# Optimization experiments

Hardware: AMD Instinct MI355X
Metric: run time of the kernel (lower is better)

Reference implementation:

```python
import jax, jax.numpy as jnp
import numpy as np

B, CI, CO = 16, 16, 16
M1, M2, M3 = 6, 6, 6
NT, NX, NY = 39, 28, 28
NXr, NYr = 14, 14  # int((n-1)/2 + 1) for n=28


def setup_inputs() -> dict:
    key = jax.random.key(0)
    ks = jax.random.split(key, 9)
    scale = 1.0 / (CI * CO)
    u = lambda k, s: scale * jax.random.uniform(k, s, dtype=jnp.float32)
    return {
        "x": jax.random.normal(ks[0], (B, CI, NT, NXr, NYr), dtype=jnp.float32),
        "wp1_re": u(ks[1], (CI, CO, M1)), "wp1_im": u(ks[2], (CI, CO, M1)),
        "wp2_re": u(ks[3], (CI, CO, M2)), "wp2_im": u(ks[4], (CI, CO, M2)),
        "wp3_re": u(ks[5], (CI, CO, M3)), "wp3_im": u(ks[6], (CI, CO, M3)),
        "wr_re": u(ks[7], (CI, CO, M1, M2, M3)), "wr_im": u(ks[8], (CI, CO, M1, M2, M3)),
    }


def _forward(x, wp1, wp2, wp3, wr):
    # grids (match torch.linspace with hardcoded nt/nx/ny and truncation)
    tt_np = np.linspace(0.0, NT - 1, NT)
    tx_np = np.linspace(0.0, 1.0, NX)[:NXr]
    ty_np = np.linspace(0.0, 1.0, NY)[:NYr]
    dtt = float(tt_np[1] - tt_np[0])
    dtx = float(tx_np[1] - tx_np[0])
    dty = float(ty_np[1] - ty_np[0])

    alpha = jnp.fft.fftn(x, axes=(-3, -2, -1))  # [B, CI, NT, NXr, NYr] complex64

    lam1 = (2j * np.pi * jnp.fft.fftfreq(NT, dtt)).astype(jnp.complex64)   # [NT]
    lam2 = (2j * np.pi * jnp.fft.fftfreq(NXr, dtx)).astype(jnp.complex64)  # [NXr]
    lam3 = (2j * np.pi * jnp.fft.fftfreq(NYr, dty)).astype(jnp.complex64)  # [NYr]

    # per-axis pole reciprocals: 1/((l1-p1)(l2-p2)(l3-p3)) = (1/(l1-p1))(1/(l2-p2))(1/(l3-p3))
    r1 = 1.0 / (lam1[:, None, None, None] - wp1[None])  # [NT,  CI, CO, M1]
    r2 = 1.0 / (lam2[:, None, None, None] - wp2[None])  # [NXr, CI, CO, M2]
    r3 = 1.0 / (lam3[:, None, None, None] - wp3[None])  # [NYr, CI, CO, M3]

    # Hw[m,n,l,i,k,p,q,r] = wr[i,k,p,q,r]*r1[m,i,k,p]*r2[n,i,k,q]*r3[l,i,k,r]
    # output_residue1[b,k,m,n,l] = sum_{i,p,q,r} alpha[b,i,m,n,l] * Hw
    or1 = jnp.einsum('bimnl,ikpqr,mikp,nikq,likr->bkmnl', alpha, wr, r1, r2, r3)
    # output_residue2[b,k,p,q,r] = -sum_{i,m,n,l} alpha[b,i,m,n,l] * Hw
    or2 = -jnp.einsum('bimnl,ikpqr,mikp,nikq,likr->bkpqr', alpha, wr, r1, r2, r3)

    x1 = jnp.real(jnp.fft.ifftn(or1, s=(NT, NXr, NYr), axes=(-3, -2, -1))).astype(jnp.float32)

    tt = jnp.asarray(tt_np, dtype=jnp.float32).astype(jnp.complex64)
    tx = jnp.asarray(tx_np, dtype=jnp.float32).astype(jnp.complex64)
    ty = jnp.asarray(ty_np, dtype=jnp.float32).astype(jnp.complex64)

    e1 = jnp.exp(wp1[..., None] * tt)  # [CI, CO, M1, NT]
    e2 = jnp.exp(wp2[..., None] * tx)  # [CI, CO, M2, NXr]
    e3 = jnp.exp(wp3[..., None] * ty)  # [CI, CO, M3, NYr]

    # x2[k,i,z,x,y] = Re( sum_{b,p,q,m} or2[k,b,p,q,m]*e1[b,i,p,z]*e2[b,i,q,x]*e3[b,i,m,y] )
    x2 = jnp.real(jnp.einsum('kbpqm,bipz,biqx,bimy->kizxy', or2, e1, e2, e3)).astype(jnp.float32)
    x2 = x2 / (NT * NXr * NYr)
    return x1 + x2


def reference(x, wp1_re, wp1_im, wp2_re, wp2_im, wp3_re, wp3_im, wr_re, wr_im):
    wp1 = jax.lax.complex(wp1_re, wp1_im)
    wp2 = jax.lax.complex(wp2_re, wp2_im)
    wp3 = jax.lax.complex(wp3_re, wp3_im)
    wr = jax.lax.complex(wr_re, wr_im)
    return _forward(x, wp1, wp2, wp3, wr)
```

## Files before the change

kernel.cpp:

```cpp
#include <hip/hip_runtime.h>

constexpr int kB  = 16;
constexpr int kC  = 16;
constexpr int kM  = 6;
constexpr int kNT = 39;
constexpr int kNX = 14;
constexpr int kNY = 14;
constexpr int kNS = kNX * kNY;
constexpr int kNF = kNT * kNS;
constexpr int kNIK = kC * kC;
constexpr int kMR = kM * kM * kM;
constexpr int kFCH = 6;
constexpr int kVS = 256;

__device__ __forceinline__ float2 cmul(float2 a, float2 b) {
    return make_float2(a.x * b.x - a.y * b.y, a.x * b.y + a.y * b.x);
}
__device__ __forceinline__ void cfma(float2& c, float2 a, float2 b) {
    c.x = fmaf(a.x, b.x, fmaf(-a.y, b.y, c.x));
    c.y = fmaf(a.x, b.y, fmaf(a.y, b.x, c.y));
}

__global__ __launch_bounds__(256) void k_init(
    const float* __restrict__ wp1_re, const float* __restrict__ wp1_im,
    const float* __restrict__ wp2_re, const float* __restrict__ wp2_im,
    const float* __restrict__ wp3_re, const float* __restrict__ wp3_im,
    float2* __restrict__ F39, float2* __restrict__ F14,
    float2* __restrict__ r1t, float2* __restrict__ r2t, float2* __restrict__ r3t,
    float2* __restrict__ e1t, float2* __restrict__ e2t, float2* __restrict__ e3t)
{
    const float PI2 = 6.283185307179586f;
    int tid = blockIdx.x * blockDim.x + threadIdx.x;
    int nth = gridDim.x * blockDim.x;

    for (int idx = tid; idx < kNT * kNT; idx += nth) {
        int m = idx / kNT, t = idx % kNT;
        float ang = -PI2 * (float)((m * t) % kNT) / (float)kNT;
        float s, c; sincosf(ang, &s, &c);
        F39[idx] = make_float2(c, s);
    }
    for (int idx = tid; idx < kNX * kNX; idx += nth) {
        int a = idx / kNX, b = idx % kNX;
        float ang = -PI2 * (float)((a * b) % kNX) / (float)kNX;
        float s, c; sincosf(ang, &s, &c);
        F14[idx] = make_float2(c, s);
    }
    for (int idx = tid; idx < kNIK * kM * kNT; idx += nth) {
        int z = idx % kNT; int ikp = idx / kNT;
        float wre = wp1_re[ikp], wim = wp1_im[ikp];
        float f = (z < 20 ? (float)z : (float)(z - kNT)) / (float)kNT;
        float w = PI2 * f;
        float dr = -wre, di = w - wim;
        float inv = 1.0f / (dr * dr + di * di);
        r1t[idx] = make_float2(dr * inv, -di * inv);
        float tt = (float)z;
        float er = expf(wre * tt);
        float s, c; sincosf(wim * tt, &s, &c);
        e1t[idx] = make_float2(er * c, er * s);
    }
    for (int idx = tid; idx < kNIK * kM * kNX; idx += nth) {
        int n = idx % kNX; int ikq = idx / kNX;
        float f = (n <= 6 ? (float)n : (float)(n - kNX)) * 27.0f / 14.0f;
        float w = PI2 * f;
        float tx = (float)n * (1.0f / 27.0f);
        {
            float wre = wp2_re[ikq], wim = wp2_im[ikq];
            float dr = -wre, di = w - wim;
            float inv = 1.0f / (dr * dr + di * di);
            r2t[idx] = make_float2(dr * inv, -di * inv);
            float er = expf(wre * tx);
            float s, c; sincosf(wim * tx, &s, &c);
            e2t[idx] = make_float2(er * c, er * s);
        }
        {
            float wre = wp3_re[ikq], wim = wp3_im[ikq];
            float dr = -wre, di = w - wim;
            float inv = 1.0f / (dr * dr + di * di);
            r3t[idx] = make_float2(dr * inv, -di * inv);
            float er = expf(wre * tx);
            float s, c; sincosf(wim * tx, &s, &c);
            e3t[idx] = make_float2(er * c, er * s);
        }
    }
}

__global__ __launch_bounds__(256) void k_dft_t_real(
    const float* __restrict__ x, const float2* __restrict__ F39, float2* __restrict__ out)
{
    int bc = blockIdx.x, mg = blockIdx.y;
    __shared__ float2 Fs[13 * kNT];
    int t = threadIdx.x;
    for (int j = t; j < 13 * kNT; j += 256)
        Fs[j] = F39[(mg * 13 + j / kNT) * kNT + (j % kNT)];
    __syncthreads();
    if (t < kNS) {
        float col[kNT];
        const float* xp = x + (size_t)bc * kNF + t;
        #pragma unroll
        for (int tt = 0; tt < kNT; ++tt) col[tt] = xp[(size_t)tt * kNS];
        for (int mi = 0; mi < 13; ++mi) {
            float2 acc = make_float2(0.f, 0.f);
            #pragma unroll
            for (int tt = 0; tt < kNT; ++tt) {
                float2 f = Fs[mi * kNT + tt];
                acc.x = fmaf(f.x, col[tt], acc.x);
                acc.y = fmaf(f.y, col[tt], acc.y);
            }
            out[((size_t)bc * kNT + mg * 13 + mi) * kNS + t] = acc;
        }
    }
}

__global__ __launch_bounds__(256) void k_idft_t(
    const float2* __restrict__ in, const float2* __restrict__ F39, float2* __restrict__ out)
{
    int bk = blockIdx.x, zg = blockIdx.y;
    __shared__ float2 Fs[13 * kNT];
    int t = threadIdx.x;
    for (int j = t; j < 13 * kNT; j += 256) {
        float2 f = F39[(zg * 13 + j / kNT) * kNT + (j % kNT)];
        f.y = -f.y;
        Fs[j] = f;
    }
    __syncthreads();
    if (t < kNS) {
        float2 col[kNT];
        const float2* ip = in + (size_t)bk * kNF + t;
        #pragma unroll
        for (int m = 0; m < kNT; ++m) col[m] = ip[(size_t)m * kNS];
        for (int zi = 0; zi < 13; ++zi) {
            float2 acc = make_float2(0.f, 0.f);
            #pragma unroll
            for (int m = 0; m < kNT; ++m) cfma(acc, Fs[zi * kNT + m], col[m]);
            out[((size_t)bk * kNT + zg * 13 + zi) * kNS + t] = acc;
        }
    }
}

__global__ __launch_bounds__(256) void k_dft_xy(
    const float2* __restrict__ in, const float2* __restrict__ F14, float2* __restrict__ out)
{
    int bm = blockIdx.x;
    __shared__ float2 tile[kNS];
    __shared__ float2 tmp[kNS];
    __shared__ float2 Fs[kNX * kNX];
    int t = threadIdx.x;
    if (t < kNS) tile[t] = in[(size_t)bm * kNS + t];
    if (t < kNX * kNX) Fs[t] = F14[t];
    __syncthreads();
    if (t < kNS) {
        int n2 = t / kNY, l = t % kNY;
        float2 acc = make_float2(0.f, 0.f);
        #pragma unroll
        for (int n = 0; n < kNX; ++n) cfma(acc, Fs[n2 * kNX + n], tile[n * kNY + l]);
        tmp[t] = acc;
    }
    __syncthreads();
    if (t < kNS) {
        int n = t / kNY, l2 = t % kNY;
        float2 acc = make_float2(0.f, 0.f);
        #pragma unroll
        for (int l = 0; l < kNY; ++l) cfma(acc, Fs[l2 * kNY + l], tmp[n * kNY + l]);
        out[(size_t)bm * kNS + t] = acc;
    }
}

__global__ __launch_bounds__(256) void k_idft_xy_final(
    const float2* __restrict__ in, const float2* __restrict__ F14, float* __restrict__ outp)
{
    int bm = blockIdx.x;
    __shared__ float2 tile[kNS];
    __shared__ float2 tmp[kNS];
    __shared__ float2 Fs[kNX * kNX];
    int t = threadIdx.x;
    if (t < kNS) tile[t] = in[(size_t)bm * kNS + t];
    if (t < kNX * kNX) { float2 f = F14[t]; f.y = -f.y; Fs[t] = f; }
    __syncthreads();
    if (t < kNS) {
        int n2 = t / kNY, l = t % kNY;
        float2 acc = make_float2(0.f, 0.f);
        #pragma unroll
        for (int n = 0; n < kNX; ++n) cfma(acc, Fs[n2 * kNX + n], tile[n * kNY + l]);
        tmp[t] = acc;
    }
    __syncthreads();
    if (t < kNS) {
        int n = t / kNY, l2 = t % kNY;
        float2 acc = make_float2(0.f, 0.f);
        #pragma unroll
        for (int l = 0; l < kNY; ++l) cfma(acc, Fs[l2 * kNY + l], tmp[n * kNY + l]);
        outp[(size_t)bm * kNS + t] += acc.x * (1.0f / 7644.0f);
    }
}

__global__ __launch_bounds__(256) void k_H(
    const float* __restrict__ wr_re, const float* __restrict__ wr_im,
    const float2* __restrict__ r1t, const float2* __restrict__ r2t,
    const float2* __restrict__ r3t, float2* __restrict__ H)
{
    int ik = blockIdx.x;
    __shared__ float2 wrs[kMR];
    __shared__ float2 r1s[kM * kNT];
    __shared__ float2 r2s[kM * kNX];
    __shared__ float2 r3s[kM * kNY];
    __shared__ float2 As[kM * kM * kNY];
    __shared__ float2 Ss[kM * kNS];
    int t = threadIdx.x;
    for (int j = t; j < kMR; j += 256)
        wrs[j] = make_float2(wr_re[ik * kMR + j], wr_im[ik * kMR + j]);
    for (int j = t; j < kM * kNT; j += 256) r1s[j] = r1t[(size_t)ik * kM * kNT + j];
    for (int j = t; j < kM * kNX; j += 256) r2s[j] = r2t[(size_t)ik * kM * kNX + j];
    for (int j = t; j < kM * kNY; j += 256) r3s[j] = r3t[(size_t)ik * kM * kNY + j];
    __syncthreads();
    for (int j = t; j < kM * kM * kNY; j += 256) {
        int l = j % kNY; int pq = j / kNY;
        float2 acc = make_float2(0.f, 0.f);
        #pragma unroll
        for (int r = 0; r < kM; ++r) cfma(acc, wrs[pq * kM + r], r3s[r * kNY + l]);
        As[j] = acc;
    }
    __syncthreads();
    for (int j = t; j < kM * kNS; j += 256) {
        int l = j % kNY; int n = (j / kNY) % kNX; int p = j / kNS;
        float2 acc = make_float2(0.f, 0.f);
        #pragma unroll
        for (int q = 0; q < kM; ++q) cfma(acc, r2s[q * kNX + n], As[(p * kM + q) * kNY + l]);
        Ss[j] = acc;
    }
    __syncthreads();
    for (int j = t; j < kNF; j += 256) {
        int m = j / kNS; int nl = j % kNS;
        float2 acc = make_float2(0.f, 0.f);
        #pragma unroll
        for (int p = 0; p < kM; ++p) cfma(acc, r1s[p * kNT + m], Ss[p * kNS + nl]);
        H[(size_t)ik * kNF + j] = acc;
    }
}

__global__ __launch_bounds__(256) void k_or1(
    const float2* __restrict__ alpha, const float2* __restrict__ H, float2* __restrict__ out)
{
    int f0 = blockIdx.x * kFCH;
    __shared__ float2 As[256 * 7 + 16];
    __shared__ float2 Hs[256 * 7 + 16];
    int t = threadIdx.x;
    {
        const float2* ap = alpha + (size_t)t * kNF + f0;
        const float2* hp = H + (size_t)t * kNF + f0;
        int base = t * 7 + (t >> 4);
        #pragma unroll
        for (int j = 0; j < kFCH; ++j) {
            As[base + j] = ap[j];
            Hs[base + j] = hp[j];
        }
    }
    __syncthreads();
    int b = t >> 4, k = t & 15;
    float2 acc[kFCH];
    #pragma unroll
    for (int j = 0; j < kFCH; ++j) acc[j] = make_float2(0.f, 0.f);
    #pragma unroll
    for (int i = 0; i < kC; ++i) {
        int ai = (b * 16 + i) * 7 + b;
        int hi = (i * 16 + k) * 7 + i;
        #pragma unroll
        for (int j = 0; j < kFCH; ++j) cfma(acc[j], As[ai + j], Hs[hi + j]);
    }
    float2* op = out + (size_t)t * kNF + f0;
    #pragma unroll
    for (int j = 0; j < kFCH; ++j) op[j] = acc[j];
}

__global__ __launch_bounds__(256) void k_or2p(
    const float2* __restrict__ alpha,
    const float* __restrict__ wr_re, const float* __restrict__ wr_im,
    const float2* __restrict__ r1t, const float2* __restrict__ r2t,
    const float2* __restrict__ r3t, float2* __restrict__ P)
{
    int blk = blockIdx.x;
    int i = blk % kC; int rest = blk / kC;
    int k = rest % kC; int pb = rest / kC;
    int b0 = 2 * pb, b1 = 2 * pb + 1;
    int ik = i * kC + k;
    __shared__ float2 r1s[kM * kNT];
    __shared__ float2 r2s[kM * kNX];
    __shared__ float2 r3s[kM * kNY];
    __shared__ float2 wrs[kMR];
    __shared__ float2 T1a[kM * kNS];
    __shared__ float2 T1b[kM * kNS];
    __shared__ float2 T2a[kM * kM * kNY];
    __shared__ float2 T2b[kM * kM * kNY];
    int t = threadIdx.x;
    for (int j = t; j < kM * kNT; j += 256) r1s[j] = r1t[(size_t)ik * kM * kNT + j];
    for (int j = t; j < kM * kNX; j += 256) r2s[j] = r2t[(size_t)ik * kM * kNX + j];
    for (int j = t; j < kM * kNY; j += 256) r3s[j] = r3t[(size_t)ik * kM * kNY + j];
    for (int j = t; j < kMR; j += 256)
        wrs[j] = make_float2(wr_re[ik * kMR + j], wr_im[ik * kMR + j]);
    __syncthreads();
    if (t < kNS) {
        float2 c0 = make_float2(0.f, 0.f), c1 = c0, c2 = c0, c3 = c0, c4 = c0, c5 = c0;
        float2 d0 = c0, d1 = c0, d2 = c0, d3 = c0, d4 = c0, d5 = c0;
        const float2* ap0 = alpha + (size_t)(b0 * kC + i) * kNF + t;
        const float2* ap1 = alpha + (size_t)(b1 * kC + i) * kNF + t;
        for (int m = 0; m < kNT; ++m) {
            float2 a0 = ap0[(size_t)m * kNS];
            float2 a1 = ap1[(size_t)m * kNS];
            float2 r;
            r = r1s[0 * kNT + m]; cfma(c0, a0, r); cfma(d0, a1, r);
            r = r1s[1 * kNT + m]; cfma(c1, a0, r); cfma(d1, a1, r);
            r = r1s[2 * kNT + m]; cfma(c2, a0, r); cfma(d2, a1, r);
            r = r1s[3 * kNT + m]; cfma(c3, a0, r); cfma(d3, a1, r);
            r = r1s[4 * kNT + m]; cfma(c4, a0, r); cfma(d4, a1, r);
            r = r1s[5 * kNT + m]; cfma(c5, a0, r); cfma(d5, a1, r);
        }
        T1a[0 * kNS + t] = c0; T1a[1 * kNS + t] = c1; T1a[2 * kNS + t] = c2;
        T1a[3 * kNS + t] = c3; T1a[4 * kNS + t] = c4; T1a[5 * kNS + t] = c5;
        T1b[0 * kNS + t] = d0; T1b[1 * kNS + t] = d1; T1b[2 * kNS + t] = d2;
        T1b[3 * kNS + t] = d3; T1b[4 * kNS + t] = d4; T1b[5 * kNS + t] = d5;
    }
    __syncthreads();
    for (int j = t; j < kM * kM * kNY; j += 256) {
        int l = j % kNY; int q = (j / kNY) % kM; int p = j / (kNY * kM);
        float2 a2 = make_float2(0.f, 0.f);
        float2 b2 = make_float2(0.f, 0.f);
        #pragma unroll
        for (int n = 0; n < kNX; ++n) {
            float2 r = r2s[q * kNX + n];
            cfma(a2, T1a[p * kNS + n * kNY + l], r);
            cfma(b2, T1b[p * kNS + n * kNY + l], r);
        }
        T2a[j] = a2;
        T2b[j] = b2;
    }
    __syncthreads();
    if (t < kMR) {
        int r = t % kM; int q = (t / kM) % kM; int p = t / (kM * kM);
        float2 t3a = make_float2(0.f, 0.f);
        float2 t3b = make_float2(0.f, 0.f);
        #pragma unroll
        for (int l = 0; l < kNY; ++l) {
            float2 rr = r3s[r * kNY + l];
            cfma(t3a, T2a[(p * kM + q) * kNY + l], rr);
            cfma(t3b, T2b[(p * kM + q) * kNY + l], rr);
        }
        float2 w = wrs[t];
        P[((size_t)(b0 * kC + k) * kC + i) * kMR + t] = cmul(w, t3a);
        P[((size_t)(b1 * kC + k) * kC + i) * kMR + t] = cmul(w, t3b);
    }
}

__global__ __launch_bounds__(256) void k_or2red(
    const float2* __restrict__ P, float2* __restrict__ or2)
{
    int id = blockIdx.x * blockDim.x + threadIdx.x;
    if (id >= kB * kC * kMR) return;
    int t = id % kMR; int bk = id / kMR;
    float2 s = make_float2(0.f, 0.f);
    #pragma unroll
    for (int i = 0; i < kC; ++i) {
        float2 v = P[((size_t)bk * kC + i) * kMR + t];
        s.x += v.x; s.y += v.y;
    }
    or2[id] = make_float2(-s.x, -s.y);
}

__global__ __launch_bounds__(256) void k_x2v(
    const float2* __restrict__ or2,
    const float2* __restrict__ e2t, const float2* __restrict__ e3t,
    float2* __restrict__ Vg)
{
    int bid = blockIdx.x;
    int c = bid & 15; int rest = bid >> 4;
    int k = rest & 15; int b = rest >> 4;
    int ck = c * kC + k;
    __shared__ float2 o2s[kMR];
    __shared__ float2 e2s[kM * kNX];
    __shared__ float2 e3s[kM * kNY];
    __shared__ float2 Us[kM * kM * kNY];
    int t = threadIdx.x;
    if (t < kMR) o2s[t] = or2[(size_t)(b * kC + c) * kMR + t];
    if (t < kM * kNX) e2s[t] = e2t[(size_t)ck * (kM * kNX) + t];
    if (t < kM * kNY) e3s[t] = e3t[(size_t)ck * (kM * kNY) + t];
    __syncthreads();
    for (int j = t; j < kM * kM * kNY; j += 256) {
        int y = j % kNY, pq = j / kNY;
        float2 u = make_float2(0.f, 0.f);
        #pragma unroll
        for (int m = 0; m < kM; ++m) cfma(u, o2s[pq * kM + m], e3s[m * kNY + y]);
        Us[j] = u;
    }
    __syncthreads();
    size_t vbase = ((size_t)(b * kC + k) * (kC * kM) + c * kM) * kVS;
    for (int j = t; j < kM * kVS; j += 256) {
        int p = j >> 8, s = j & 255;
        float2 v = make_float2(0.f, 0.f);
        if (s < kNS) {
            int x = s / kNY, y = s % kNY;
            #pragma unroll
            for (int q = 0; q < kM; ++q)
                cfma(v, Us[(p * kM + q) * kNY + y], e2s[q * kNX + x]);
        }
        Vg[vbase + (size_t)p * kVS + s] = v;
    }
}

__global__ __launch_bounds__(256) void k_x2gemm(
    const float2* __restrict__ Vg, const float2* __restrict__ e1t,
    float* __restrict__ outp)
{
    int bx = blockIdx.x;
    int bk = bx & 255, zc = bx >> 8;
    int k = bk & 15;
    int z0 = zc * 13;
    __shared__ float2 e1w[96 * 16];
    __shared__ float2 Vs[2][8 * kVS];
    int t = threadIdx.x;
    for (int j = t; j < 96 * 16; j += 256) {
        int row = j >> 4, zi = j & 15;
        int c = row / kM, p = row % kM;
        float2 e = make_float2(0.f, 0.f);
        if (zi < 13)
            e = e1t[((size_t)(c * kC + k) * kM + p) * kNT + z0 + zi];
        e1w[j] = e;
    }

    int sl = t & 63, zt = t >> 6;
    const float2* vpan = Vg + (size_t)bk * (kC * kM) * kVS;
    #pragma unroll
    for (int j = 0; j < 8; ++j) Vs[0][j * 256 + t] = vpan[j * 256 + t];
    __syncthreads();

    float acc[4][4];
    #pragma unroll
    for (int zi = 0; zi < 4; ++zi)
        #pragma unroll
        for (int j = 0; j < 4; ++j) acc[zi][j] = 0.f;

    for (int ch = 0; ch < 12; ++ch) {
        int cur = ch & 1;
        if (ch + 1 < 12) {
            const float2* src = vpan + (size_t)(ch + 1) * 8 * kVS;
            #pragma unroll
            for (int j = 0; j < 8; ++j) Vs[cur ^ 1][j * 256 + t] = src[j * 256 + t];
        }
        #pragma unroll
        for (int r = 0; r < 8; ++r) {
            int kk = ch * 8 + r;
            float2 vr[4];
            #pragma unroll
            for (int j = 0; j < 4; ++j) vr[j] = Vs[cur][r * 256 + sl + 64 * j];
            const int e1base = kk * 16 + zt;
            #pragma unroll
            for (int zi = 0; zi < 4; ++zi) {
                float2 e = e1w[e1base + 4 * zi];
                #pragma unroll
                for (int j = 0; j < 4; ++j)
                    acc[zi][j] = fmaf(vr[j].x, e.x, fmaf(-vr[j].y, e.y, acc[zi][j]));
            }
        }
        __syncthreads();
    }

    const float sc = 1.0f / 7644.0f;
    size_t base = (size_t)bk * kNF;
    #pragma unroll
    for (int zi = 0; zi < 4; ++zi) {
        int zloc = zt + 4 * zi;
        if (zloc < 13) {
            size_t zb = base + (size_t)(z0 + zloc) * kNS;
            #pragma unroll
            for (int j = 0; j < 4; ++j) {
                int s = sl + 64 * j;
                if (s < kNS) outp[zb + s] = acc[zi][j] * sc;
            }
        }
    }
}

extern "C" void kernel_launch(void* const* d_in, const int* in_sizes, int n_in,
                              void* d_out, int out_size, void* d_ws, size_t ws_size,
                              hipStream_t stream) {
    (void)in_sizes; (void)n_in; (void)out_size; (void)ws_size;
    const float* x      = (const float*)d_in[0];
    const float* wp1_re = (const float*)d_in[1];
    const float* wp1_im = (const float*)d_in[2];
    const float* wp2_re = (const float*)d_in[3];
    const float* wp2_im = (const float*)d_in[4];
    const float* wp3_re = (const float*)d_in[5];
    const float* wp3_im = (const float*)d_in[6];
    const float* wr_re  = (const float*)d_in[7];
    const float* wr_im  = (const float*)d_in[8];
    float* out = (float*)d_out;

    const size_t big = (size_t)kNIK * kNF;
    float2* A   = (float2*)d_ws;
    float2* Bb  = A + big;
    float2* Cc  = Bb + big;
    float2* OR2 = Cc + big;
    float2* r1t = OR2 + (size_t)kB * kC * kMR;
    float2* r2t = r1t + (size_t)kNIK * kM * kNT;
    float2* r3t = r2t + (size_t)kNIK * kM * kNX;
    float2* e1t = r3t + (size_t)kNIK * kM * kNY;
    float2* e2t = e1t + (size_t)kNIK * kM * kNT;
    float2* e3t = e2t + (size_t)kNIK * kM * kNX;
    float2* F39 = e3t + (size_t)kNIK * kM * kNY;
    float2* F14 = F39 + kNT * kNT;
    float2* Vg  = F14 + kNX * kNX;

    k_init<<<64, 256, 0, stream>>>(wp1_re, wp1_im, wp2_re, wp2_im, wp3_re, wp3_im,
                                   F39, F14, r1t, r2t, r3t, e1t, e2t, e3t);
    k_dft_t_real<<<dim3(kNIK, 3), 256, 0, stream>>>(x, F39, A);
    k_dft_xy<<<kNIK * kNT, 256, 0, stream>>>(A, F14, Bb);
    k_H<<<kNIK, 256, 0, stream>>>(wr_re, wr_im, r1t, r2t, r3t, Cc);
    k_or1<<<kNF / kFCH, 256, 0, stream>>>(Bb, Cc, A);
    k_or2p<<<(kB / 2) * kC * kC, 256, 0, stream>>>(Bb, wr_re, wr_im, r1t, r2t, r3t, Cc);
    k_or2red<<<(kB * kC * kMR + 255) / 256, 256, 0, stream>>>(Cc, OR2);
    k_x2v<<<kB * kC * kC, 256, 0, stream>>>(OR2, e2t, e3t, Vg);
    k_x2gemm<<<kB * kC * 3, 256, 0, stream>>>(Vg, e1t, out);
    k_idft_t<<<dim3(kB * kC, 3), 256, 0, stream>>>(A, F39, Cc);
    k_idft_xy_final<<<kNIK * kNT, 256, 0, stream>>>(Cc, F14, out);
}
```

Before: 191.9 us.

## Fuse t-axis and xy DFT passes and split x2 GEMM reduction

Merges the time-axis DFT with the 2D xy DFT in both forward and inverse directions, so each block transforms its 13 time slices through shared memory without a global intermediate round trip. This removes two kernels and their big buffer traffic. The x2 GEMM is split over two halves of the reduction dimension to double the block count, with a new reduction kernel summing the partials. In exchange the fused kernels have only 768 blocks with extra barriers per slice, and the split adds a partial-buffer write plus an extra pass.

```diff
diff --git a/kernel.cpp b/kernel.cpp
--- a/kernel.cpp
+++ b/kernel.cpp
@@ -84,21 +84,31 @@
     }
 }
 
-__global__ __launch_bounds__(256) void k_dft_t_real(
-    const float* __restrict__ x, const float2* __restrict__ F39, float2* __restrict__ out)
+__global__ __launch_bounds__(256) void k_dft_fwd(
+    const float* __restrict__ x, const float2* __restrict__ F39,
+    const float2* __restrict__ F14, float2* __restrict__ alpha)
 {
     int bc = blockIdx.x, mg = blockIdx.y;
     __shared__ float2 Fs[13 * kNT];
+    __shared__ float2 F14s[kNX * kNX];
+    __shared__ float2 tile[kNS];
+    __shared__ float2 tmp[kNS];
     int t = threadIdx.x;
     for (int j = t; j < 13 * kNT; j += 256)
         Fs[j] = F39[(mg * 13 + j / kNT) * kNT + (j % kNT)];
-    __syncthreads();
+    for (int j = t; j < kNX * kNX; j += 256) F14s[j] = F14[j];
+
+    float col[kNT];
     if (t < kNS) {
-        float col[kNT];
         const float* xp = x + (size_t)bc * kNF + t;
         #pragma unroll
         for (int tt = 0; tt < kNT; ++tt) col[tt] = xp[(size_t)tt * kNS];
-        for (int mi = 0; mi < 13; ++mi) {
+    }
+    __syncthreads();
+
+    int n2 = t / kNY, l = t % kNY;
+    for (int mi = 0; mi < 13; ++mi) {
+        if (t < kNS) {
             float2 acc = make_float2(0.f, 0.f);
             #pragma unroll
             for (int tt = 0; tt < kNT; ++tt) {
@@ -106,90 +116,77 @@
                 acc.x = fmaf(f.x, col[tt], acc.x);
                 acc.y = fmaf(f.y, col[tt], acc.y);
             }
-            out[((size_t)bc * kNT + mg * 13 + mi) * kNS + t] = acc;
-        }
-    }
-}
-
-__global__ __launch_bounds__(256) void k_idft_t(
-    const float2* __restrict__ in, const float2* __restrict__ F39, float2* __restrict__ out)
+            tile[t] = acc;
+        }
+        __syncthreads();
+        if (t < kNS) {
+            float2 acc = make_float2(0.f, 0.f);
+            #pragma unroll
+            for (int n = 0; n < kNX; ++n) cfma(acc, F14s[n2 * kNX + n], tile[n * kNY + l]);
+            tmp[t] = acc;
+        }
+        __syncthreads();
+        if (t < kNS) {
+            float2 acc = make_float2(0.f, 0.f);
+            #pragma unroll
+            for (int ll = 0; ll < kNY; ++ll) cfma(acc, F14s[l * kNY + ll], tmp[n2 * kNY + ll]);
+            alpha[((size_t)bc * kNT + mg * 13 + mi) * kNS + t] = acc;
+        }
+        __syncthreads();
+    }
+}
+
+__global__ __launch_bounds__(256) void k_idft_fused(
+    const float2* __restrict__ in, const float2* __restrict__ F39,
+    const float2* __restrict__ F14, float* __restrict__ outp)
 {
     int bk = blockIdx.x, zg = blockIdx.y;
     __shared__ float2 Fs[13 * kNT];
+    __shared__ float2 F14s[kNX * kNX];
+    __shared__ float2 tile[kNS];
+    __shared__ float2 tmp[kNS];
     int t = threadIdx.x;
     for (int j = t; j < 13 * kNT; j += 256) {
         float2 f = F39[(zg * 13 + j / kNT) * kNT + (j % kNT)];
         f.y = -f.y;
         Fs[j] = f;
     }
-    __syncthreads();
+    for (int j = t; j < kNX * kNX; j += 256) {
+        float2 f = F14[j]; f.y = -f.y; F14s[j] = f;
+    }
+
+    float2 col[kNT];
     if (t < kNS) {
-        float2 col[kNT];
         const float2* ip = in + (size_t)bk * kNF + t;
         #pragma unroll
         for (int m = 0; m < kNT; ++m) col[m] = ip[(size_t)m * kNS];
-        for (int zi = 0; zi < 13; ++zi) {
+    }
+    __syncthreads();
+
+    int n2 = t / kNY, l = t % kNY;
+    const float sc = 1.0f / 7644.0f;
+    for (int zi = 0; zi < 13; ++zi) {
+        if (t < kNS) {
             float2 acc = make_float2(0.f, 0.f);
             #pragma unroll
             for (int m = 0; m < kNT; ++m) cfma(acc, Fs[zi * kNT + m], col[m]);
-            out[((size_t)bk * kNT + zg * 13 + zi) * kNS + t] = acc;
-        }
-    }
-}
-
-__global__ __launch_bounds__(256) void k_dft_xy(
-    const float2* __restrict__ in, const float2* __restrict__ F14, float2* __restrict__ out)
-{
-    int bm = blockIdx.x;
-    __shared__ float2 tile[kNS];
-    __shared__ float2 tmp[kNS];
-    __shared__ float2 Fs[kNX * kNX];
-    int t = threadIdx.x;
-    if (t < kNS) tile[t] = in[(size_t)bm * kNS + t];
-    if (t < kNX * kNX) Fs[t] = F14[t];
-    __syncthreads();
-    if (t < kNS) {
-        int n2 = t / kNY, l = t % kNY;
-        float2 acc = make_float2(0.f, 0.f);
-        #pragma unroll
-        for (int n = 0; n < kNX; ++n) cfma(acc, Fs[n2 * kNX + n], tile[n * kNY + l]);
-        tmp[t] = acc;
-    }
-    __syncthreads();
-    if (t < kNS) {
-        int n = t / kNY, l2 = t % kNY;
-        float2 acc = make_float2(0.f, 0.f);
-        #pragma unroll
-        for (int l = 0; l < kNY; ++l) cfma(acc, Fs[l2 * kNY + l], tmp[n * kNY + l]);
-        out[(size_t)bm * kNS + t] = acc;
-    }
-}
-
-__global__ __launch_bounds__(256) void k_idft_xy_final(
-    const float2* __restrict__ in, const float2* __restrict__ F14, float* __restrict__ outp)
-{
-    int bm = blockIdx.x;
-    __shared__ float2 tile[kNS];
-    __shared__ float2 tmp[kNS];
-    __shared__ float2 Fs[kNX * kNX];
-    int t = threadIdx.x;
-    if (t < kNS) tile[t] = in[(size_t)bm * kNS + t];
-    if (t < kNX * kNX) { float2 f = F14[t]; f.y = -f.y; Fs[t] = f; }
-    __syncthreads();
-    if (t < kNS) {
-        int n2 = t / kNY, l = t % kNY;
-        float2 acc = make_float2(0.f, 0.f);
-        #pragma unroll
-        for (int n = 0; n < kNX; ++n) cfma(acc, Fs[n2 * kNX + n], tile[n * kNY + l]);
-        tmp[t] = acc;
-    }
-    __syncthreads();
-    if (t < kNS) {
-        int n = t / kNY, l2 = t % kNY;
-        float2 acc = make_float2(0.f, 0.f);
-        #pragma unroll
-        for (int l = 0; l < kNY; ++l) cfma(acc, Fs[l2 * kNY + l], tmp[n * kNY + l]);
-        outp[(size_t)bm * kNS + t] += acc.x * (1.0f / 7644.0f);
+            tile[t] = acc;
+        }
+        __syncthreads();
+        if (t < kNS) {
+            float2 acc = make_float2(0.f, 0.f);
+            #pragma unroll
+            for (int n = 0; n < kNX; ++n) cfma(acc, F14s[n2 * kNX + n], tile[n * kNY + l]);
+            tmp[t] = acc;
+        }
+        __syncthreads();
+        if (t < kNS) {
+            float2 acc = make_float2(0.f, 0.f);
+            #pragma unroll
+            for (int ll = 0; ll < kNY; ++ll) cfma(acc, F14s[l * kNY + ll], tmp[n2 * kNY + ll]);
+            outp[((size_t)bk * kNT + zg * 13 + zi) * kNS + t] += acc.x * sc;
+        }
+        __syncthreads();
     }
 }
 
@@ -406,18 +403,21 @@
 
 __global__ __launch_bounds__(256) void k_x2gemm(
     const float2* __restrict__ Vg, const float2* __restrict__ e1t,
-    float* __restrict__ outp)
+    float* __restrict__ P2)
 {
     int bx = blockIdx.x;
-    int bk = bx & 255, zc = bx >> 8;
+    int bk = bx & 255;
+    int zckh = bx >> 8;
+    int kh = zckh / 3, zc = zckh % 3;
     int k = bk & 15;
     int z0 = zc * 13;
-    __shared__ float2 e1w[96 * 16];
-    __shared__ float2 Vs[2][8 * kVS];
-    int t = threadIdx.x;
-    for (int j = t; j < 96 * 16; j += 256) {
+    __shared__ float2 e1w[48 * 16];
+    __shared__ float2 Vs[2][4 * kVS];
+    int t = threadIdx.x;
+    for (int j = t; j < 48 * 16; j += 256) {
         int row = j >> 4, zi = j & 15;
-        int c = row / kM, p = row % kM;
+        int cp = kh * 48 + row;
+        int c = cp / kM, p = cp % kM;
         float2 e = make_float2(0.f, 0.f);
         if (zi < 13)
             e = e1t[((size_t)(c * kC + k) * kM + p) * kNT + z0 + zi];
@@ -425,9 +425,9 @@
     }
 
     int sl = t & 63, zt = t >> 6;
-    const float2* vpan = Vg + (size_t)bk * (kC * kM) * kVS;
-    #pragma unroll
-    for (int j = 0; j < 8; ++j) Vs[0][j * 256 + t] = vpan[j * 256 + t];
+    const float2* vpan = Vg + (size_t)bk * (kC * kM) * kVS + (size_t)kh * 48 * kVS;
+    #pragma unroll
+    for (int j = 0; j < 4; ++j) Vs[0][j * 256 + t] = vpan[j * 256 + t];
     __syncthreads();
 
     float acc[4][4];
@@ -439,17 +439,17 @@
     for (int ch = 0; ch < 12; ++ch) {
         int cur = ch & 1;
         if (ch + 1 < 12) {
-            const float2* src = vpan + (size_t)(ch + 1) * 8 * kVS;
-            #pragma unroll
-            for (int j = 0; j < 8; ++j) Vs[cur ^ 1][j * 256 + t] = src[j * 256 + t];
-        }
-        #pragma unroll
-        for (int r = 0; r < 8; ++r) {
-            int kk = ch * 8 + r;
+            const float2* src = vpan + (size_t)(ch + 1) * 4 * kVS;
+            #pragma unroll
+            for (int j = 0; j < 4; ++j) Vs[cur ^ 1][j * 256 + t] = src[j * 256 + t];
+        }
+        #pragma unroll
+        for (int r = 0; r < 4; ++r) {
+            int row = ch * 4 + r;
             float2 vr[4];
             #pragma unroll
             for (int j = 0; j < 4; ++j) vr[j] = Vs[cur][r * 256 + sl + 64 * j];
-            const int e1base = kk * 16 + zt;
+            const int e1base = row * 16 + zt;
             #pragma unroll
             for (int zi = 0; zi < 4; ++zi) {
                 float2 e = e1w[e1base + 4 * zi];
@@ -461,8 +461,7 @@
         __syncthreads();
     }
 
-    const float sc = 1.0f / 7644.0f;
-    size_t base = (size_t)bk * kNF;
+    size_t base = ((size_t)kh * kNIK + bk) * kNF;
     #pragma unroll
     for (int zi = 0; zi < 4; ++zi) {
         int zloc = zt + 4 * zi;
@@ -471,10 +470,19 @@
             #pragma unroll
             for (int j = 0; j < 4; ++j) {
                 int s = sl + 64 * j;
-                if (s < kNS) outp[zb + s] = acc[zi][j] * sc;
+                if (s < kNS) P2[zb + s] = acc[zi][j];
             }
         }
     }
+}
+
+__global__ __launch_bounds__(256) void k_x2red(
+    const float* __restrict__ P2, float* __restrict__ outp)
+{
+    int id = blockIdx.x * blockDim.x + threadIdx.x;
+    if (id >= kNIK * kNF) return;
+    const float sc = 1.0f / 7644.0f;
+    outp[id] = (P2[id] + P2[(size_t)kNIK * kNF + id]) * sc;
 }
 
 extern "C" void kernel_launch(void* const* d_in, const int* in_sizes, int n_in,
@@ -509,14 +517,13 @@
 
     k_init<<<64, 256, 0, stream>>>(wp1_re, wp1_im, wp2_re, wp2_im, wp3_re, wp3_im,
                                    F39, F14, r1t, r2t, r3t, e1t, e2t, e3t);
-    k_dft_t_real<<<dim3(kNIK, 3), 256, 0, stream>>>(x, F39, A);
-    k_dft_xy<<<kNIK * kNT, 256, 0, stream>>>(A, F14, Bb);
+    k_dft_fwd<<<dim3(kNIK, 3), 256, 0, stream>>>(x, F39, F14, Bb);
     k_H<<<kNIK, 256, 0, stream>>>(wr_re, wr_im, r1t, r2t, r3t, Cc);
     k_or1<<<kNF / kFCH, 256, 0, stream>>>(Bb, Cc, A);
     k_or2p<<<(kB / 2) * kC * kC, 256, 0, stream>>>(Bb, wr_re, wr_im, r1t, r2t, r3t, Cc);
     k_or2red<<<(kB * kC * kMR + 255) / 256, 256, 0, stream>>>(Cc, OR2);
     k_x2v<<<kB * kC * kC, 256, 0, stream>>>(OR2, e2t, e3t, Vg);
-    k_x2gemm<<<kB * kC * 3, 256, 0, stream>>>(Vg, e1t, out);
-    k_idft_t<<<dim3(kB * kC, 3), 256, 0, stream>>>(A, F39, Cc);
-    k_idft_xy_final<<<kNIK * kNT, 256, 0, stream>>>(Cc, F14, out);
-}
+    k_x2gemm<<<kB * kC * 6, 256, 0, stream>>>(Vg, e1t, (float*)Cc);
+    k_x2red<<<(int)((big + 255) / 256), 256, 0, stream>>>((const float*)Cc, out);
+    k_idft_fused<<<dim3(kB * kC, 3), 256, 0, stream>>>(A, F39, F14, out);
+}
```

Result: faster. 186.1 us (-3.0%).
